# Performance work log

Measured on AMD Instinct MI355X. Metric: run time of the kernel, lower is better.

The kernel has to match this reference:

```python
import jax, jax.numpy as jnp
import numpy as np

N, E, F, H, L = 100000, 800000, 128, 128, 64


def _glorot(key, shape):
    lim = float(np.sqrt(6.0 / (shape[0] + shape[1])))
    return jax.random.uniform(key, shape, jnp.float32, -lim, lim)


def setup_inputs() -> dict:
    key = jax.random.key(0)
    ks = jax.random.split(key, 10)
    x = jax.random.normal(ks[0], (N, F), jnp.float32)
    noise = jax.random.normal(ks[1], (N, F), jnp.float32)
    edge_index = jax.random.randint(ks[2], (2, E), 0, N, jnp.int32)
    return {
        "x": x,
        "noise": noise,
        "edge_index": edge_index,
        "bn_gamma": jnp.ones((F,), jnp.float32),
        "bn_beta": jnp.zeros((F,), jnp.float32),
        "W1": _glorot(ks[3], (F, H)),
        "b1": jnp.zeros((H,), jnp.float32),
        "W2": _glorot(ks[4], (H + 2 * F, H)),
        "b2": jnp.zeros((H,), jnp.float32),
        "Wm": _glorot(ks[5], (H + F, L)),
        "bm": jnp.zeros((L,), jnp.float32),
        "Ws": _glorot(ks[6], (H + F, L)),
        "bs": jnp.zeros((L,), jnp.float32),
    }


def _gcn_conv(x, W, b, src, dst, norm, n):
    # GCNConv: transform, then sym-normalized sparse aggregation, then bias
    h = x @ W                                 # [n, out]
    msg = h[src] * norm[:, None]              # gather + scale  [E', out]
    return jax.ops.segment_sum(msg, dst, num_segments=n) + b


def reference(x, noise, edge_index, bn_gamma, bn_beta, W1, b1, W2, b2, Wm, bm, Ws, bs):
    n = x.shape[0]
    loops = jnp.arange(n, dtype=edge_index.dtype)
    src = jnp.concatenate([edge_index[0], loops])  # add self-loops
    dst = jnp.concatenate([edge_index[1], loops])
    deg = jax.ops.segment_sum(jnp.ones_like(src, dtype=x.dtype), dst, num_segments=n)
    dinv = jnp.where(deg > 0, jax.lax.rsqrt(jnp.maximum(deg, 1e-12)), 0.0)
    norm = dinv[src] * dinv[dst]                   # D^-1/2 A D^-1/2 edge weights

    # bn1 (training-mode batch norm over nodes)
    mu = x.mean(axis=0)
    var = x.var(axis=0)
    xb = (x - mu) * jax.lax.rsqrt(var + 1e-5) * bn_gamma + bn_beta

    h1 = jax.nn.relu(_gcn_conv(xb, W1, b1, src, dst, norm, n))
    h1 = jnp.concatenate([xb, noise, h1], axis=1)  # [n, H + 2F]
    h2 = jax.nn.relu(_gcn_conv(h1, W2, b2, src, dst, norm, n))
    # dropout(p=0.4) in eval mode -> identity
    last = jnp.concatenate([xb, h2], axis=1)       # [n, F + H]
    z_mean = _gcn_conv(last, Wm, bm, src, dst, norm, n)
    z_logstd = _gcn_conv(last, Ws, bs, src, dst, norm, n)
    return (z_mean, z_logstd)
```

## Files before the change

kernel.cpp:

```cpp
#include <hip/hip_runtime.h>
#include <math.h>


typedef short bf16x8 __attribute__((ext_vector_type(8)));
typedef float f32x4 __attribute__((ext_vector_type(4)));
typedef float f32x2 __attribute__((ext_vector_type(2)));

#define BN_G 1024
#define SCAN_BLK 256
#define SCAN_ELEMS 1024

__device__ inline unsigned short f2bf(float f) {
    unsigned int u = __builtin_bit_cast(unsigned int, f);
    u += 0x7fff + ((u >> 16) & 1);
    return (unsigned short)(u >> 16);
}
__device__ inline unsigned int pack2(float lo, float hi) {
    return ((unsigned int)f2bf(hi) << 16) | f2bf(lo);
}
__device__ inline f32x2 unp(unsigned int u) {
    return (f32x2){__builtin_bit_cast(float, u << 16),
                   __builtin_bit_cast(float, u & 0xffff0000u)};
}
__device__ inline void acc8v(f32x2* a, uint4 v) {
    a[0] += unp(v.x); a[1] += unp(v.y); a[2] += unp(v.z); a[3] += unp(v.w);
}

__device__ __forceinline__ void gload_lds16(const void* g, void* l) {
    __builtin_amdgcn_global_load_lds(
        (const __attribute__((address_space(1))) unsigned int*)g,
        (__attribute__((address_space(3))) unsigned int*)l, 16, 0, 0);
}

__global__ __launch_bounds__(256) void fused1(const float4* __restrict__ x4,
                                              float* __restrict__ partials, int n,
                                              const int* __restrict__ ei,
                                              int* __restrict__ cnt,
                                              int* __restrict__ slot, int E) {
    __shared__ float4 lds[2][8][32];
    int bid = blockIdx.x, t = threadIdx.x;
    if (bid < BN_G) {
        int cg = t & 31;
        int rs = t >> 5;
        float4 s = make_float4(0.f, 0.f, 0.f, 0.f);
        float4 q = make_float4(0.f, 0.f, 0.f, 0.f);
        const float4 z4 = make_float4(0.f, 0.f, 0.f, 0.f);
        const int stride = BN_G * 32;
        for (int r0 = bid * 32 + rs * 4; r0 < n; r0 += stride) {
            float4 v0 = x4[(size_t)r0 * 32 + cg];
            float4 v1 = (r0 + 1 < n) ? x4[(size_t)(r0 + 1) * 32 + cg] : z4;
            float4 v2 = (r0 + 2 < n) ? x4[(size_t)(r0 + 2) * 32 + cg] : z4;
            float4 v3 = (r0 + 3 < n) ? x4[(size_t)(r0 + 3) * 32 + cg] : z4;
            s.x += v0.x + v1.x + v2.x + v3.x;
            s.y += v0.y + v1.y + v2.y + v3.y;
            s.z += v0.z + v1.z + v2.z + v3.z;
            s.w += v0.w + v1.w + v2.w + v3.w;
            q.x = fmaf(v0.x, v0.x, fmaf(v1.x, v1.x, fmaf(v2.x, v2.x, fmaf(v3.x, v3.x, q.x))));
            q.y = fmaf(v0.y, v0.y, fmaf(v1.y, v1.y, fmaf(v2.y, v2.y, fmaf(v3.y, v3.y, q.y))));
            q.z = fmaf(v0.z, v0.z, fmaf(v1.z, v1.z, fmaf(v2.z, v2.z, fmaf(v3.z, v3.z, q.z))));
            q.w = fmaf(v0.w, v0.w, fmaf(v1.w, v1.w, fmaf(v2.w, v2.w, fmaf(v3.w, v3.w, q.w))));
        }
        lds[0][rs][cg] = s;
        lds[1][rs][cg] = q;
        __syncthreads();
        if (t < 64) {
            int which = t >> 5;
            int c = t & 31;
            float4 a = lds[which][0][c];
#pragma unroll
            for (int i = 1; i < 8; i++) {
                float4 b = lds[which][i][c];
                a.x += b.x; a.y += b.y; a.z += b.z; a.w += b.w;
            }
            int base = which * 128 + c * 4;
            partials[(size_t)(base + 0) * BN_G + bid] = a.x;
            partials[(size_t)(base + 1) * BN_G + bid] = a.y;
            partials[(size_t)(base + 2) * BN_G + bid] = a.z;
            partials[(size_t)(base + 3) * BN_G + bid] = a.w;
        }
        return;
    }
    int e = (bid - BN_G) * 256 + t;
    if (e < E) slot[e] = atomicAdd(&cnt[ei[E + e]], 1);
}

__global__ __launch_bounds__(256) void fused2(const float4* __restrict__ partials4,
                                              float* __restrict__ stats,
                                              const int* __restrict__ cnt,
                                              int* __restrict__ row_ptr,
                                              int* __restrict__ bsums, int n) {
    __shared__ float red[256];
    __shared__ int lds[SCAN_BLK];
    int t = threadIdx.x;
    if (blockIdx.x < 256) {
        int c = blockIdx.x;
        float4 v = partials4[(size_t)c * (BN_G / 4) + t];
        red[t] = v.x + v.y + v.z + v.w;
        __syncthreads();
        for (int off = 128; off > 0; off >>= 1) {
            if (t < off) red[t] += red[t + off];
            __syncthreads();
        }
        if (t == 0) stats[c] = red[0];
    } else {
        int blk = blockIdx.x - 256;
        int base = blk * SCAN_ELEMS;
        int v[4];
        int s = 0;
#pragma unroll
        for (int j = 0; j < 4; j++) {
            int i = base + t * 4 + j;
            v[j] = s;
            s += (i < n) ? cnt[i] : 0;
        }
        lds[t] = s;
        __syncthreads();
        for (int off = 1; off < SCAN_BLK; off <<= 1) {
            int val = (t >= off) ? lds[t - off] : 0;
            __syncthreads();
            lds[t] += val;
            __syncthreads();
        }
        int excl = (t == 0) ? 0 : lds[t - 1];
#pragma unroll
        for (int j = 0; j < 4; j++) {
            int i = base + t * 4 + j;
            if (i < n) row_ptr[i] = excl + v[j];
        }
        if (t == SCAN_BLK - 1) bsums[blk] = lds[t];
    }
}

__global__ void fused3(int* __restrict__ bsums, int nb,
                       const float* __restrict__ stats,
                       const float* __restrict__ gamma, const float* __restrict__ beta,
                       float* __restrict__ scale, float* __restrict__ shift, float invN) {
    int t = threadIdx.x;
    if (t == 0) {
        int acc = 0;
        for (int i = 0; i < nb; i++) { int c = bsums[i]; bsums[i] = acc; acc += c; }
    } else if (t >= 128 && t < 256) {
        int c = t - 128;
        float mu = stats[c] * invN;
        float var = stats[128 + c] * invN - mu * mu;
        float sc = gamma[c] / sqrtf(var + 1e-5f);
        scale[c] = sc;
        shift[c] = beta[c] - mu * sc;
    }
}

__global__ void fused4(int* __restrict__ row_ptr, const int* __restrict__ bsums,
                       const int* __restrict__ cnt, float* __restrict__ dinv,
                       int n, int E) {
    int i = blockIdx.x * blockDim.x + threadIdx.x;
    if (i < n) {
        row_ptr[i] += bsums[i / SCAN_ELEMS];
        dinv[i] = rsqrtf((float)cnt[i] + 1.0f);
    }
    if (i == 0) row_ptr[n] = E;
}

__device__ inline void pack_body(int i, const float* __restrict__ W,
                                 unsigned short* __restrict__ Wp,
                                 int K, int C, int colOff) {
    if (i >= K * C) return;
    int k = i / C, c = i % C;
    int gc = c + colOff;
    int s = k >> 7, kc = (k >> 5) & 3, lhi = (k >> 3) & 3, j = k & 7;
    int wc = gc >> 6, n = (gc >> 4) & 3, l15 = gc & 15;
    int lane = lhi * 16 + l15;
    size_t dst = ((size_t)((s * 2 + wc) * 4 + kc) * 4 + n) * 512 + lane * 8 + j;
    Wp[dst] = f2bf(W[i]);
}

__global__ __launch_bounds__(256) void fused5(
    const int* __restrict__ ei, const int* __restrict__ row_ptr,
    const int* __restrict__ slot, int* __restrict__ edge_src, int E, int EB,
    const float4* __restrict__ x4, const float4* __restrict__ n4,
    const float* __restrict__ scale, const float* __restrict__ shift,
    ushort4* __restrict__ xb, ushort4* __restrict__ nb4, int total4, int CB,
    const float* __restrict__ W1, unsigned short* __restrict__ Wp1,
    const float* __restrict__ W2, unsigned short* __restrict__ Wp2,
    const float* __restrict__ Wm, const float* __restrict__ Ws,
    unsigned short* __restrict__ Wpc)
{
    int bid = blockIdx.x, t = threadIdx.x;
    if (bid < EB) {
        int e = bid * 256 + t;
        if (e < E) {
            int s = ei[e], d = ei[E + e];
            edge_src[row_ptr[d] + slot[e]] = s;
        }
        return;
    }
    bid -= EB;
    if (bid < CB) {
        int i = bid * 256 + t;
        if (i < total4) {
            int c4 = (i & 31) << 2;
            float4 sc = *reinterpret_cast<const float4*>(scale + c4);
            float4 sh = *reinterpret_cast<const float4*>(shift + c4);
            float4 v = x4[i];
            ushort4 o;
            o.x = f2bf(fmaf(v.x, sc.x, sh.x));
            o.y = f2bf(fmaf(v.y, sc.y, sh.y));
            o.z = f2bf(fmaf(v.z, sc.z, sh.z));
            o.w = f2bf(fmaf(v.w, sc.w, sh.w));
            xb[i] = o;
            float4 w = n4[i];
            ushort4 p;
            p.x = f2bf(w.x); p.y = f2bf(w.y); p.z = f2bf(w.z); p.w = f2bf(w.w);
            nb4[i] = p;
        }
        return;
    }
    bid -= CB;
    if (bid < 64)  { pack_body(bid * 256 + t, W1, Wp1, 128, 128, 0); return; }
    bid -= 64;
    if (bid < 192) { pack_body(bid * 256 + t, W2, Wp2, 384, 128, 0); return; }
    bid -= 192;
    if (bid < 64)  { pack_body(bid * 256 + t, Wm, Wpc, 256, 64, 0); return; }
    bid -= 64;
    pack_body(bid * 256 + t, Ws, Wpc, 256, 64, 64);
}

template <int NSRC>
__global__ __launch_bounds__(256, 4) void gemm_mfma(
    const unsigned short* __restrict__ A0, const unsigned short* __restrict__ A1,
    const unsigned short* __restrict__ A2,
    const unsigned short* __restrict__ Wpk,
    const float* __restrict__ dinv, unsigned short* __restrict__ out)
{
    constexpr int NBUF = (NSRC > 1) ? 2 : 1;
    __shared__ unsigned char ldsA[NBUF][64 * 256];

    const int lane = threadIdx.x & 63;
    const int wid  = threadIdx.x >> 6;
    const int wr   = wid >> 1, wc = wid & 1;
    const int l15  = lane & 15, lhi = lane >> 4;
    const int c0   = wc * 64;
    const long rowblk = (long)blockIdx.x * 64;
    const int rl0 = wr * 32 + l15;
    const int rl1 = rl0 + 16;
    const int rsw = rl0 & 7;

    const unsigned short* __restrict__ srcs[3] = {A0, A1, A2};
    auto stage = [&](int s, int b) {
#pragma unroll
        for (int i = 0; i < 4; i++) {
            int G = (wid * 4 + i) * 64 + lane;
            int r = G >> 4, g = G & 15;
            const unsigned short* src = srcs[s] + (rowblk + r) * 128 + (g ^ (r & 7)) * 8;
            gload_lds16(src, &ldsA[b][G * 16]);
        }
    };

    f32x4 acc[2][4];
#pragma unroll
    for (int g = 0; g < 2; g++)
#pragma unroll
        for (int n = 0; n < 4; n++)
            acc[g][n] = (f32x4){0.f, 0.f, 0.f, 0.f};

    stage(0, 0);

#pragma unroll
    for (int s = 0; s < NSRC; s++) {
        const unsigned short* wbase = Wpk + ((size_t)(s * 2 + wc) * 16) * 512 + lane * 8;
        bf16x8 w[4][4];
#pragma unroll
        for (int kc = 0; kc < 4; kc++)
#pragma unroll
            for (int n = 0; n < 4; n++)
                w[kc][n] = *reinterpret_cast<const bf16x8*>(wbase + (kc * 4 + n) * 512);

        __syncthreads();
        if (s + 1 < NSRC) stage(s + 1, (s + 1) % NBUF);
        const unsigned char* bufp = ldsA[s % NBUF];

#pragma unroll
        for (int kc = 0; kc < 4; kc++) {
            int g0 = kc * 4 + lhi;
            bf16x8 a0 = *reinterpret_cast<const bf16x8*>(bufp + rl0 * 256 + (g0 ^ rsw) * 16);
            bf16x8 a1 = *reinterpret_cast<const bf16x8*>(bufp + rl1 * 256 + (g0 ^ rsw) * 16);
#pragma unroll
            for (int n = 0; n < 4; n++) {
                acc[0][n] = __builtin_amdgcn_mfma_f32_16x16x32_bf16(w[kc][n], a0, acc[0][n], 0, 0, 0);
                acc[1][n] = __builtin_amdgcn_mfma_f32_16x16x32_bf16(w[kc][n], a1, acc[1][n], 0, 0, 0);
            }
        }
    }

#pragma unroll
    for (int g = 0; g < 2; g++) {
        long row = rowblk + (g ? rl1 : rl0);
        float dv = dinv[row];
        unsigned short* op = out + row * 128 + c0 + lhi * 4;
#pragma unroll
        for (int n = 0; n < 4; n++) {
            f32x4 v = acc[g][n];
            ushort4 pk;
            pk.x = f2bf(v[0] * dv);
            pk.y = f2bf(v[1] * dv);
            pk.z = f2bf(v[2] * dv);
            pk.w = f2bf(v[3] * dv);
            *reinterpret_cast<ushort4*>(op + n * 16) = pk;
        }
    }
}

template <bool RELU>
__global__ void gather16(const uint4* __restrict__ hs4, const float* __restrict__ dinv,
                         const int* __restrict__ row_ptr, const int* __restrict__ edge_src,
                         const float* __restrict__ bias, uint4* __restrict__ out4, int n) {
    int node = blockIdx.x * 16 + (threadIdx.x >> 4);
    if (node >= n) return;
    int cl = threadIdx.x & 15;
    int beg = row_ptr[node], end = row_ptr[node + 1];
    f32x2 a[4] = {(f32x2){0.f,0.f}, (f32x2){0.f,0.f}, (f32x2){0.f,0.f}, (f32x2){0.f,0.f}};
    f32x2 b[4] = {(f32x2){0.f,0.f}, (f32x2){0.f,0.f}, (f32x2){0.f,0.f}, (f32x2){0.f,0.f}};
    acc8v(a, hs4[(size_t)node * 16 + cl]);
    int e = beg;
    for (; e + 4 <= end; e += 4) {
        uint4 v0 = hs4[(size_t)edge_src[e] * 16 + cl];
        uint4 v1 = hs4[(size_t)edge_src[e + 1] * 16 + cl];
        uint4 v2 = hs4[(size_t)edge_src[e + 2] * 16 + cl];
        uint4 v3 = hs4[(size_t)edge_src[e + 3] * 16 + cl];
        acc8v(a, v0);
        acc8v(b, v1);
        acc8v(a, v2);
        acc8v(b, v3);
    }
    if (e + 2 <= end) {
        uint4 v0 = hs4[(size_t)edge_src[e] * 16 + cl];
        uint4 v1 = hs4[(size_t)edge_src[e + 1] * 16 + cl];
        acc8v(a, v0);
        acc8v(b, v1);
        e += 2;
    }
    if (e < end) acc8v(a, hs4[(size_t)edge_src[e] * 16 + cl]);
#pragma unroll
    for (int i = 0; i < 4; i++) a[i] += b[i];
    float dv = dinv[node];
    float4 b0 = *reinterpret_cast<const float4*>(bias + cl * 8);
    float4 b1 = *reinterpret_cast<const float4*>(bias + cl * 8 + 4);
    float r0 = fmaf(a[0].x, dv, b0.x), r1 = fmaf(a[0].y, dv, b0.y);
    float r2 = fmaf(a[1].x, dv, b0.z), r3 = fmaf(a[1].y, dv, b0.w);
    float r4 = fmaf(a[2].x, dv, b1.x), r5 = fmaf(a[2].y, dv, b1.y);
    float r6 = fmaf(a[3].x, dv, b1.z), r7 = fmaf(a[3].y, dv, b1.w);
    if (RELU) {
        r0 = fmaxf(r0, 0.f); r1 = fmaxf(r1, 0.f); r2 = fmaxf(r2, 0.f); r3 = fmaxf(r3, 0.f);
        r4 = fmaxf(r4, 0.f); r5 = fmaxf(r5, 0.f); r6 = fmaxf(r6, 0.f); r7 = fmaxf(r7, 0.f);
    }
    uint4 o;
    o.x = pack2(r0, r1); o.y = pack2(r2, r3);
    o.z = pack2(r4, r5); o.w = pack2(r6, r7);
    out4[(size_t)node * 16 + cl] = o;
}

__global__ void gather_dual(const uint4* __restrict__ hs4, const float* __restrict__ dinv,
                            const int* __restrict__ row_ptr, const int* __restrict__ edge_src,
                            const float* __restrict__ bm, const float* __restrict__ bs,
                            float* __restrict__ zm, float* __restrict__ zs, int n) {
    int node = blockIdx.x * 16 + (threadIdx.x >> 4);
    if (node >= n) return;
    int cl = threadIdx.x & 15;
    int beg = row_ptr[node], end = row_ptr[node + 1];
    f32x2 a[4] = {(f32x2){0.f,0.f}, (f32x2){0.f,0.f}, (f32x2){0.f,0.f}, (f32x2){0.f,0.f}};
    f32x2 b[4] = {(f32x2){0.f,0.f}, (f32x2){0.f,0.f}, (f32x2){0.f,0.f}, (f32x2){0.f,0.f}};
    acc8v(a, hs4[(size_t)node * 16 + cl]);
    int e = beg;
    for (; e + 4 <= end; e += 4) {
        uint4 v0 = hs4[(size_t)edge_src[e] * 16 + cl];
        uint4 v1 = hs4[(size_t)edge_src[e + 1] * 16 + cl];
        uint4 v2 = hs4[(size_t)edge_src[e + 2] * 16 + cl];
        uint4 v3 = hs4[(size_t)edge_src[e + 3] * 16 + cl];
        acc8v(a, v0);
        acc8v(b, v1);
        acc8v(a, v2);
        acc8v(b, v3);
    }
    if (e + 2 <= end) {
        uint4 v0 = hs4[(size_t)edge_src[e] * 16 + cl];
        uint4 v1 = hs4[(size_t)edge_src[e + 1] * 16 + cl];
        acc8v(a, v0);
        acc8v(b, v1);
        e += 2;
    }
    if (e < end) acc8v(a, hs4[(size_t)edge_src[e] * 16 + cl]);
#pragma unroll
    for (int i = 0; i < 4; i++) a[i] += b[i];
    float dv = dinv[node];
    const float* bp = (cl < 8) ? (bm + cl * 8) : (bs + (cl - 8) * 8);
    float* zp = (cl < 8) ? (zm + (size_t)node * 64 + cl * 8)
                         : (zs + (size_t)node * 64 + (cl - 8) * 8);
    float4 b0 = *reinterpret_cast<const float4*>(bp);
    float4 b1 = *reinterpret_cast<const float4*>(bp + 4);
    float4 o0 = make_float4(fmaf(a[0].x, dv, b0.x), fmaf(a[0].y, dv, b0.y),
                            fmaf(a[1].x, dv, b0.z), fmaf(a[1].y, dv, b0.w));
    float4 o1 = make_float4(fmaf(a[2].x, dv, b1.x), fmaf(a[2].y, dv, b1.y),
                            fmaf(a[3].x, dv, b1.z), fmaf(a[3].y, dv, b1.w));
    *reinterpret_cast<float4*>(zp) = o0;
    *reinterpret_cast<float4*>(zp + 4) = o1;
}


extern "C" void kernel_launch(void* const* d_in, const int* in_sizes, int n_in,
                              void* d_out, int out_size, void* d_ws, size_t ws_size,
                              hipStream_t stream) {
    const float* x     = (const float*)d_in[0];
    const float* noise = (const float*)d_in[1];
    const int*   ei    = (const int*)d_in[2];
    const float* gamma = (const float*)d_in[3];
    const float* beta  = (const float*)d_in[4];
    const float* W1    = (const float*)d_in[5];
    const float* b1    = (const float*)d_in[6];
    const float* W2    = (const float*)d_in[7];
    const float* b2    = (const float*)d_in[8];
    const float* Wm    = (const float*)d_in[9];
    const float* bm    = (const float*)d_in[10];
    const float* Ws    = (const float*)d_in[11];
    const float* bs    = (const float*)d_in[12];

    const int N  = in_sizes[0] / 128;
    const int E  = in_sizes[2] / 2;
    const int NPAD = (N + 127) & ~127;
    const int nb = (N + SCAN_ELEMS - 1) / SCAN_ELEMS;
    const int EB = (E + 255) / 256;
    const int CB = (N * 32 + 255) / 256;

    auto align256 = [](size_t b) { return (b + 255) & ~(size_t)255; };
    char* p = (char*)d_ws;
    int* cnt      = (int*)p;  p += align256((size_t)N * 4);
    int* row_ptr  = (int*)p;  p += align256((size_t)(N + 1) * 4);
    int* edge_src = (int*)p;  p += align256((size_t)E * 4);
    int* slot     = (int*)p;  p += align256((size_t)E * 4);
    int* bsums    = (int*)p;  p += align256((size_t)nb * 4);
    float* dinv   = (float*)p; p += align256((size_t)NPAD * 4);
    float* stats  = (float*)p; p += align256(512 * 4);
    float* bnpart = (float*)p; p += align256((size_t)256 * BN_G * 4);
    unsigned short* Wp1 = (unsigned short*)p; p += align256(128 * 128 * 2);
    unsigned short* Wp2 = (unsigned short*)p; p += align256(128 * 384 * 2);
    unsigned short* Wpc = (unsigned short*)p; p += align256(128 * 256 * 2);
    unsigned short* xb16 = (unsigned short*)p; p += align256((size_t)NPAD * 128 * 2);
    unsigned short* n16  = (unsigned short*)p; p += align256((size_t)NPAD * 128 * 2);
    unsigned short* h16  = (unsigned short*)p; p += align256((size_t)NPAD * 128 * 2);

    float* scale = stats + 256;
    float* shift = stats + 384;

    float* dout = (float*)d_out;
    unsigned short* hs12 = (unsigned short*)d_out;
    unsigned short* hs3  = n16;
    float* zm = dout;
    float* zs = dout + (size_t)N * 64;

    const int gblocks = NPAD / 64;
    const int nblocks16 = (N + 15) / 16;

    hipMemsetAsync(cnt, 0, (size_t)N * 4, stream);
    fused1<<<BN_G + EB, 256, 0, stream>>>((const float4*)x, bnpart, N, ei, cnt, slot, E);
    fused2<<<256 + nb, 256, 0, stream>>>((const float4*)bnpart, stats, cnt, row_ptr, bsums, N);
    fused3<<<1, 256, 0, stream>>>(bsums, nb, stats, gamma, beta, scale, shift, 1.0f / (float)N);
    fused4<<<(N + 255) / 256, 256, 0, stream>>>(row_ptr, bsums, cnt, dinv, N, E);
    fused5<<<EB + CB + 384, 256, 0, stream>>>(
        ei, row_ptr, slot, edge_src, E, EB,
        (const float4*)x, (const float4*)noise, scale, shift,
        (ushort4*)xb16, (ushort4*)n16, N * 32, CB,
        W1, Wp1, W2, Wp2, Wm, Ws, Wpc);

    gemm_mfma<1><<<gblocks, 256, 0, stream>>>(xb16, nullptr, nullptr, Wp1, dinv, hs12);
    gather16<true><<<nblocks16, 256, 0, stream>>>((const uint4*)hs12, dinv, row_ptr,
                                                  edge_src, b1, (uint4*)h16, N);
    gemm_mfma<3><<<gblocks, 256, 0, stream>>>(xb16, n16, h16, Wp2, dinv, hs12);
    gather16<true><<<nblocks16, 256, 0, stream>>>((const uint4*)hs12, dinv, row_ptr,
                                                  edge_src, b2, (uint4*)h16, N);
    gemm_mfma<2><<<gblocks, 256, 0, stream>>>(xb16, h16, nullptr, Wpc, dinv, hs3);
    gather_dual<<<nblocks16, 256, 0, stream>>>((const uint4*)hs3, dinv, row_ptr,
                                               edge_src, bm, bs, zm, zs, N);
}
```

Before: 272.6 us.

## Fuse sparse gather aggregation into following GEMM via LDS staging

Replaces the standalone gather16 kernels with a gather_gemm kernel. Each block first aggregates neighbor rows for its 64 nodes, applying bias and ReLU, and writes the result into swizzled LDS. It then feeds that tile directly into the MFMA GEMM with the other dense inputs. This removes a global-memory round trip of the intermediate h activations and two kernel launches. In exchange, the gather runs with only 64 rows per block, one thread group per four nodes serially, and higher LDS use, which may limit occupancy and latency hiding for the irregular gather.

```diff
diff --git a/kernel.cpp b/kernel.cpp
--- a/kernel.cpp
+++ b/kernel.cpp
@@ -309,53 +309,147 @@
     }
 }
 
-template <bool RELU>
-__global__ void gather16(const uint4* __restrict__ hs4, const float* __restrict__ dinv,
-                         const int* __restrict__ row_ptr, const int* __restrict__ edge_src,
-                         const float* __restrict__ bias, uint4* __restrict__ out4, int n) {
-    int node = blockIdx.x * 16 + (threadIdx.x >> 4);
-    if (node >= n) return;
-    int cl = threadIdx.x & 15;
-    int beg = row_ptr[node], end = row_ptr[node + 1];
-    f32x2 a[4] = {(f32x2){0.f,0.f}, (f32x2){0.f,0.f}, (f32x2){0.f,0.f}, (f32x2){0.f,0.f}};
-    f32x2 b[4] = {(f32x2){0.f,0.f}, (f32x2){0.f,0.f}, (f32x2){0.f,0.f}, (f32x2){0.f,0.f}};
-    acc8v(a, hs4[(size_t)node * 16 + cl]);
-    int e = beg;
-    for (; e + 4 <= end; e += 4) {
-        uint4 v0 = hs4[(size_t)edge_src[e] * 16 + cl];
-        uint4 v1 = hs4[(size_t)edge_src[e + 1] * 16 + cl];
-        uint4 v2 = hs4[(size_t)edge_src[e + 2] * 16 + cl];
-        uint4 v3 = hs4[(size_t)edge_src[e + 3] * 16 + cl];
-        acc8v(a, v0);
-        acc8v(b, v1);
-        acc8v(a, v2);
-        acc8v(b, v3);
-    }
-    if (e + 2 <= end) {
-        uint4 v0 = hs4[(size_t)edge_src[e] * 16 + cl];
-        uint4 v1 = hs4[(size_t)edge_src[e + 1] * 16 + cl];
-        acc8v(a, v0);
-        acc8v(b, v1);
-        e += 2;
-    }
-    if (e < end) acc8v(a, hs4[(size_t)edge_src[e] * 16 + cl]);
-#pragma unroll
-    for (int i = 0; i < 4; i++) a[i] += b[i];
-    float dv = dinv[node];
-    float4 b0 = *reinterpret_cast<const float4*>(bias + cl * 8);
-    float4 b1 = *reinterpret_cast<const float4*>(bias + cl * 8 + 4);
-    float r0 = fmaf(a[0].x, dv, b0.x), r1 = fmaf(a[0].y, dv, b0.y);
-    float r2 = fmaf(a[1].x, dv, b0.z), r3 = fmaf(a[1].y, dv, b0.w);
-    float r4 = fmaf(a[2].x, dv, b1.x), r5 = fmaf(a[2].y, dv, b1.y);
-    float r6 = fmaf(a[3].x, dv, b1.z), r7 = fmaf(a[3].y, dv, b1.w);
-    if (RELU) {
-        r0 = fmaxf(r0, 0.f); r1 = fmaxf(r1, 0.f); r2 = fmaxf(r2, 0.f); r3 = fmaxf(r3, 0.f);
-        r4 = fmaxf(r4, 0.f); r5 = fmaxf(r5, 0.f); r6 = fmaxf(r6, 0.f); r7 = fmaxf(r7, 0.f);
-    }
-    uint4 o;
-    o.x = pack2(r0, r1); o.y = pack2(r2, r3);
-    o.z = pack2(r4, r5); o.w = pack2(r6, r7);
-    out4[(size_t)node * 16 + cl] = o;
+template <int NG>
+__global__ __launch_bounds__(256, 3) void gather_gemm(
+    const unsigned short* __restrict__ A0, const unsigned short* __restrict__ A1,
+    const uint4* __restrict__ hsrc,
+    const float* __restrict__ dinv, const int* __restrict__ row_ptr,
+    const int* __restrict__ edge_src, const float* __restrict__ gbias,
+    const unsigned short* __restrict__ Wpk,
+    unsigned short* __restrict__ out, int n)
+{
+    constexpr int NSRC = NG + 1;
+    __shared__ unsigned char ldsA[NG][64 * 256];
+    __shared__ uint4 hlds[64 * 16];
+
+    const int t = threadIdx.x;
+    const int lane = t & 63;
+    const int wid  = t >> 6;
+    const int wr   = wid >> 1, wc = wid & 1;
+    const int l15  = lane & 15, lhi = lane >> 4;
+    const int c0   = wc * 64;
+    const long rowblk = (long)blockIdx.x * 64;
+    const int rl0 = wr * 32 + l15;
+    const int rl1 = rl0 + 16;
+    const int rsw = rl0 & 7;
+
+    const unsigned short* __restrict__ srcs[2] = {A0, A1};
+    auto stage = [&](int s, int b) {
+#pragma unroll
+        for (int i = 0; i < 4; i++) {
+            int G = (wid * 4 + i) * 64 + lane;
+            int r = G >> 4, g = G & 15;
+            const unsigned short* src = srcs[s] + (rowblk + r) * 128 + (g ^ (r & 7)) * 8;
+            gload_lds16(src, &ldsA[b][G * 16]);
+        }
+    };
+
+    stage(0, 0);
+
+    {
+        int grp = t >> 4, cl = t & 15;
+#pragma unroll
+        for (int i = 0; i < 4; i++) {
+            int r = grp * 4 + i;
+            long node = rowblk + r;
+            uint4 o = make_uint4(0u, 0u, 0u, 0u);
+            if (node < n) {
+                int beg = row_ptr[node], end = row_ptr[node + 1];
+                f32x2 a[4] = {(f32x2){0.f,0.f}, (f32x2){0.f,0.f},
+                              (f32x2){0.f,0.f}, (f32x2){0.f,0.f}};
+                f32x2 ab[4] = {(f32x2){0.f,0.f}, (f32x2){0.f,0.f},
+                               (f32x2){0.f,0.f}, (f32x2){0.f,0.f}};
+                acc8v(a, hsrc[(size_t)node * 16 + cl]);
+                int e = beg;
+                for (; e + 4 <= end; e += 4) {
+                    uint4 v0 = hsrc[(size_t)edge_src[e] * 16 + cl];
+                    uint4 v1 = hsrc[(size_t)edge_src[e + 1] * 16 + cl];
+                    uint4 v2 = hsrc[(size_t)edge_src[e + 2] * 16 + cl];
+                    uint4 v3 = hsrc[(size_t)edge_src[e + 3] * 16 + cl];
+                    acc8v(a, v0);
+                    acc8v(ab, v1);
+                    acc8v(a, v2);
+                    acc8v(ab, v3);
+                }
+                if (e + 2 <= end) {
+                    uint4 v0 = hsrc[(size_t)edge_src[e] * 16 + cl];
+                    uint4 v1 = hsrc[(size_t)edge_src[e + 1] * 16 + cl];
+                    acc8v(a, v0);
+                    acc8v(ab, v1);
+                    e += 2;
+                }
+                if (e < end) acc8v(a, hsrc[(size_t)edge_src[e] * 16 + cl]);
+#pragma unroll
+                for (int j = 0; j < 4; j++) a[j] += ab[j];
+                float dv = dinv[node];
+                float4 b0 = *reinterpret_cast<const float4*>(gbias + cl * 8);
+                float4 b1 = *reinterpret_cast<const float4*>(gbias + cl * 8 + 4);
+                float r0 = fmaxf(fmaf(a[0].x, dv, b0.x), 0.f);
+                float r1 = fmaxf(fmaf(a[0].y, dv, b0.y), 0.f);
+                float r2 = fmaxf(fmaf(a[1].x, dv, b0.z), 0.f);
+                float r3 = fmaxf(fmaf(a[1].y, dv, b0.w), 0.f);
+                float r4 = fmaxf(fmaf(a[2].x, dv, b1.x), 0.f);
+                float r5 = fmaxf(fmaf(a[2].y, dv, b1.y), 0.f);
+                float r6 = fmaxf(fmaf(a[3].x, dv, b1.z), 0.f);
+                float r7 = fmaxf(fmaf(a[3].y, dv, b1.w), 0.f);
+                o.x = pack2(r0, r1); o.y = pack2(r2, r3);
+                o.z = pack2(r4, r5); o.w = pack2(r6, r7);
+            }
+            hlds[r * 16 + (cl ^ (r & 7))] = o;
+        }
+    }
+
+    f32x4 acc[2][4];
+#pragma unroll
+    for (int g = 0; g < 2; g++)
+#pragma unroll
+        for (int n = 0; n < 4; n++)
+            acc[g][n] = (f32x4){0.f, 0.f, 0.f, 0.f};
+
+#pragma unroll
+    for (int s = 0; s < NSRC; s++) {
+        const unsigned short* wbase = Wpk + ((size_t)(s * 2 + wc) * 16) * 512 + lane * 8;
+        bf16x8 w[4][4];
+#pragma unroll
+        for (int kc = 0; kc < 4; kc++)
+#pragma unroll
+            for (int n = 0; n < 4; n++)
+                w[kc][n] = *reinterpret_cast<const bf16x8*>(wbase + (kc * 4 + n) * 512);
+
+        __syncthreads();
+        if (s + 1 < NG) stage(s + 1, s + 1);
+        const unsigned char* bufp = (s < NG) ? ldsA[s]
+                                             : reinterpret_cast<const unsigned char*>(hlds);
+
+#pragma unroll
+        for (int kc = 0; kc < 4; kc++) {
+            int g0 = kc * 4 + lhi;
+            bf16x8 a0 = *reinterpret_cast<const bf16x8*>(bufp + rl0 * 256 + (g0 ^ rsw) * 16);
+            bf16x8 a1 = *reinterpret_cast<const bf16x8*>(bufp + rl1 * 256 + (g0 ^ rsw) * 16);
+#pragma unroll
+            for (int n = 0; n < 4; n++) {
+                acc[0][n] = __builtin_amdgcn_mfma_f32_16x16x32_bf16(w[kc][n], a0, acc[0][n], 0, 0, 0);
+                acc[1][n] = __builtin_amdgcn_mfma_f32_16x16x32_bf16(w[kc][n], a1, acc[1][n], 0, 0, 0);
+            }
+        }
+    }
+
+#pragma unroll
+    for (int g = 0; g < 2; g++) {
+        long row = rowblk + (g ? rl1 : rl0);
+        float dv = dinv[row];
+        unsigned short* op = out + row * 128 + c0 + lhi * 4;
+#pragma unroll
+        for (int n = 0; n < 4; n++) {
+            f32x4 v = acc[g][n];
+            ushort4 pk;
+            pk.x = f2bf(v[0] * dv);
+            pk.y = f2bf(v[1] * dv);
+            pk.z = f2bf(v[2] * dv);
+            pk.w = f2bf(v[3] * dv);
+            *reinterpret_cast<ushort4*>(op + n * 16) = pk;
+        }
+    }
 }
 
 __global__ void gather_dual(const uint4* __restrict__ hs4, const float* __restrict__ dinv,
@@ -451,7 +545,6 @@
 
     float* dout = (float*)d_out;
     unsigned short* hs12 = (unsigned short*)d_out;
-    unsigned short* hs3  = n16;
     float* zm = dout;
     float* zs = dout + (size_t)N * 64;
 
@@ -469,13 +562,11 @@
         (ushort4*)xb16, (ushort4*)n16, N * 32, CB,
         W1, Wp1, W2, Wp2, Wm, Ws, Wpc);
 
-    gemm_mfma<1><<<gblocks, 256, 0, stream>>>(xb16, nullptr, nullptr, Wp1, dinv, hs12);
-    gather16<true><<<nblocks16, 256, 0, stream>>>((const uint4*)hs12, dinv, row_ptr,
-                                                  edge_src, b1, (uint4*)h16, N);
-    gemm_mfma<3><<<gblocks, 256, 0, stream>>>(xb16, n16, h16, Wp2, dinv, hs12);
-    gather16<true><<<nblocks16, 256, 0, stream>>>((const uint4*)hs12, dinv, row_ptr,
-                                                  edge_src, b2, (uint4*)h16, N);
-    gemm_mfma<2><<<gblocks, 256, 0, stream>>>(xb16, h16, nullptr, Wpc, dinv, hs3);
-    gather_dual<<<nblocks16, 256, 0, stream>>>((const uint4*)hs3, dinv, row_ptr,
+    gemm_mfma<1><<<gblocks, 256, 0, stream>>>(xb16, nullptr, nullptr, Wp1, dinv, h16);
+    gather_gemm<2><<<gblocks, 256, 0, stream>>>(
+        xb16, n16, (const uint4*)h16, dinv, row_ptr, edge_src, b1, Wp2, hs12, N);
+    gather_gemm<1><<<gblocks, 256, 0, stream>>>(
+        xb16, nullptr, (const uint4*)hs12, dinv, row_ptr, edge_src, b2, Wpc, h16, N);
+    gather_dual<<<nblocks16, 256, 0, stream>>>((const uint4*)h16, dinv, row_ptr,
                                                edge_src, bm, bs, zm, zs, N);
 }
```

Measured after the change: 293.5 us. +7.7%, slower.

## Fold batch-norm affine into weights and GEMM epilogue; convert raw x early

Applied to the files above, without the earlier changes.

Batch-norm scale is folded into the rows of each packed weight matrix that multiply the xb block. The shift term becomes a per-column bias vector (shift·W), computed by three extra blocks and added in the GEMM epilogue. Raw x is converted to bf16 inside the stats pass while it is already loaded, so the later pass that re-read x in fp32 to normalize it is removed. The cost is rounding the unnormalized x to bf16 instead of the normalized values, which may shift precision, plus extra stores in the stats kernel.

```diff
diff --git a/kernel.cpp b/kernel.cpp
--- a/kernel.cpp
+++ b/kernel.cpp
@@ -25,6 +25,11 @@
 __device__ inline void acc8v(f32x2* a, uint4 v) {
     a[0] += unp(v.x); a[1] += unp(v.y); a[2] += unp(v.z); a[3] += unp(v.w);
 }
+__device__ inline ushort4 cvt4(float4 v) {
+    ushort4 o;
+    o.x = f2bf(v.x); o.y = f2bf(v.y); o.z = f2bf(v.z); o.w = f2bf(v.w);
+    return o;
+}
 
 __device__ __forceinline__ void gload_lds16(const void* g, void* l) {
     __builtin_amdgcn_global_load_lds(
@@ -34,6 +39,7 @@
 
 __global__ __launch_bounds__(256) void fused1(const float4* __restrict__ x4,
                                               float* __restrict__ partials, int n,
+                                              ushort4* __restrict__ x16,
                                               const int* __restrict__ ei,
                                               int* __restrict__ cnt,
                                               int* __restrict__ slot, int E) {
@@ -51,6 +57,10 @@
             float4 v1 = (r0 + 1 < n) ? x4[(size_t)(r0 + 1) * 32 + cg] : z4;
             float4 v2 = (r0 + 2 < n) ? x4[(size_t)(r0 + 2) * 32 + cg] : z4;
             float4 v3 = (r0 + 3 < n) ? x4[(size_t)(r0 + 3) * 32 + cg] : z4;
+            x16[(size_t)r0 * 32 + cg] = cvt4(v0);
+            if (r0 + 1 < n) x16[(size_t)(r0 + 1) * 32 + cg] = cvt4(v1);
+            if (r0 + 2 < n) x16[(size_t)(r0 + 2) * 32 + cg] = cvt4(v2);
+            if (r0 + 3 < n) x16[(size_t)(r0 + 3) * 32 + cg] = cvt4(v3);
             s.x += v0.x + v1.x + v2.x + v3.x;
             s.y += v0.y + v1.y + v2.y + v3.y;
             s.z += v0.z + v1.z + v2.z + v3.z;
@@ -162,28 +172,32 @@
 
 __device__ inline void pack_body(int i, const float* __restrict__ W,
                                  unsigned short* __restrict__ Wp,
-                                 int K, int C, int colOff) {
+                                 int K, int C, int colOff,
+                                 const float* __restrict__ scale) {
     if (i >= K * C) return;
     int k = i / C, c = i % C;
+    float v = W[i];
+    if (k < 128) v *= scale[k];
     int gc = c + colOff;
     int s = k >> 7, kc = (k >> 5) & 3, lhi = (k >> 3) & 3, j = k & 7;
     int wc = gc >> 6, n = (gc >> 4) & 3, l15 = gc & 15;
     int lane = lhi * 16 + l15;
     size_t dst = ((size_t)((s * 2 + wc) * 4 + kc) * 4 + n) * 512 + lane * 8 + j;
-    Wp[dst] = f2bf(W[i]);
+    Wp[dst] = f2bf(v);
 }
 
 __global__ __launch_bounds__(256) void fused5(
     const int* __restrict__ ei, const int* __restrict__ row_ptr,
     const int* __restrict__ slot, int* __restrict__ edge_src, int E, int EB,
-    const float4* __restrict__ x4, const float4* __restrict__ n4,
+    const float4* __restrict__ n4, ushort4* __restrict__ nb4, int total4, int CB,
     const float* __restrict__ scale, const float* __restrict__ shift,
-    ushort4* __restrict__ xb, ushort4* __restrict__ nb4, int total4, int CB,
     const float* __restrict__ W1, unsigned short* __restrict__ Wp1,
     const float* __restrict__ W2, unsigned short* __restrict__ Wp2,
     const float* __restrict__ Wm, const float* __restrict__ Ws,
-    unsigned short* __restrict__ Wpc)
+    unsigned short* __restrict__ Wpc,
+    float* __restrict__ cv1, float* __restrict__ cv2, float* __restrict__ cvc)
 {
+    __shared__ float cred[256];
     int bid = blockIdx.x, t = threadIdx.x;
     if (bid < EB) {
         int e = bid * 256 + t;
@@ -196,32 +210,41 @@
     bid -= EB;
     if (bid < CB) {
         int i = bid * 256 + t;
-        if (i < total4) {
-            int c4 = (i & 31) << 2;
-            float4 sc = *reinterpret_cast<const float4*>(scale + c4);
-            float4 sh = *reinterpret_cast<const float4*>(shift + c4);
-            float4 v = x4[i];
-            ushort4 o;
-            o.x = f2bf(fmaf(v.x, sc.x, sh.x));
-            o.y = f2bf(fmaf(v.y, sc.y, sh.y));
-            o.z = f2bf(fmaf(v.z, sc.z, sh.z));
-            o.w = f2bf(fmaf(v.w, sc.w, sh.w));
-            xb[i] = o;
-            float4 w = n4[i];
-            ushort4 p;
-            p.x = f2bf(w.x); p.y = f2bf(w.y); p.z = f2bf(w.z); p.w = f2bf(w.w);
-            nb4[i] = p;
-        }
+        if (i < total4) nb4[i] = cvt4(n4[i]);
         return;
     }
     bid -= CB;
-    if (bid < 64)  { pack_body(bid * 256 + t, W1, Wp1, 128, 128, 0); return; }
+    if (bid < 64)  { pack_body(bid * 256 + t, W1, Wp1, 128, 128, 0, scale); return; }
     bid -= 64;
-    if (bid < 192) { pack_body(bid * 256 + t, W2, Wp2, 384, 128, 0); return; }
+    if (bid < 192) { pack_body(bid * 256 + t, W2, Wp2, 384, 128, 0, scale); return; }
     bid -= 192;
-    if (bid < 64)  { pack_body(bid * 256 + t, Wm, Wpc, 256, 64, 0); return; }
+    if (bid < 64)  { pack_body(bid * 256 + t, Wm, Wpc, 256, 64, 0, scale); return; }
     bid -= 64;
-    pack_body(bid * 256 + t, Ws, Wpc, 256, 64, 64);
+    if (bid < 64)  { pack_body(bid * 256 + t, Ws, Wpc, 256, 64, 64, scale); return; }
+    bid -= 64;
+    {
+        int c = t & 127, kh = t >> 7;
+        float s = 0.f;
+        if (bid == 0) {
+            for (int k = kh * 64; k < kh * 64 + 64; k++)
+                s = fmaf(shift[k], W1[k * 128 + c], s);
+        } else if (bid == 1) {
+            for (int k = kh * 64; k < kh * 64 + 64; k++)
+                s = fmaf(shift[k], W2[k * 128 + c], s);
+        } else {
+            const float* Wsrc = (c < 64) ? Wm : Ws;
+            int cc = (c < 64) ? c : c - 64;
+            for (int k = kh * 64; k < kh * 64 + 64; k++)
+                s = fmaf(shift[k], Wsrc[k * 64 + cc], s);
+        }
+        cred[t] = s;
+        __syncthreads();
+        if (t < 128) {
+            float v = cred[t] + cred[t + 128];
+            float* dst = (bid == 0) ? cv1 : (bid == 1) ? cv2 : cvc;
+            dst[c] = v;
+        }
+    }
 }
 
 template <int NSRC>
@@ -229,7 +252,8 @@
     const unsigned short* __restrict__ A0, const unsigned short* __restrict__ A1,
     const unsigned short* __restrict__ A2,
     const unsigned short* __restrict__ Wpk,
-    const float* __restrict__ dinv, unsigned short* __restrict__ out)
+    const float* __restrict__ dinv, const float* __restrict__ cvec,
+    unsigned short* __restrict__ out)
 {
     constexpr int NBUF = (NSRC > 1) ? 2 : 1;
     __shared__ unsigned char ldsA[NBUF][64 * 256];
@@ -291,6 +315,11 @@
         }
     }
 
+    float4 cv[4];
+#pragma unroll
+    for (int n = 0; n < 4; n++)
+        cv[n] = *reinterpret_cast<const float4*>(cvec + c0 + n * 16 + lhi * 4);
+
 #pragma unroll
     for (int g = 0; g < 2; g++) {
         long row = rowblk + (g ? rl1 : rl0);
@@ -300,10 +329,10 @@
         for (int n = 0; n < 4; n++) {
             f32x4 v = acc[g][n];
             ushort4 pk;
-            pk.x = f2bf(v[0] * dv);
-            pk.y = f2bf(v[1] * dv);
-            pk.z = f2bf(v[2] * dv);
-            pk.w = f2bf(v[3] * dv);
+            pk.x = f2bf((v[0] + cv[n].x) * dv);
+            pk.y = f2bf((v[1] + cv[n].y) * dv);
+            pk.z = f2bf((v[2] + cv[n].z) * dv);
+            pk.w = f2bf((v[3] + cv[n].w) * dv);
             *reinterpret_cast<ushort4*>(op + n * 16) = pk;
         }
     }
@@ -438,13 +467,16 @@
     int* bsums    = (int*)p;  p += align256((size_t)nb * 4);
     float* dinv   = (float*)p; p += align256((size_t)NPAD * 4);
     float* stats  = (float*)p; p += align256(512 * 4);
+    float* cv1    = (float*)p; p += align256(128 * 4);
+    float* cv2    = (float*)p; p += align256(128 * 4);
+    float* cvc    = (float*)p; p += align256(128 * 4);
     float* bnpart = (float*)p; p += align256((size_t)256 * BN_G * 4);
     unsigned short* Wp1 = (unsigned short*)p; p += align256(128 * 128 * 2);
     unsigned short* Wp2 = (unsigned short*)p; p += align256(128 * 384 * 2);
     unsigned short* Wpc = (unsigned short*)p; p += align256(128 * 256 * 2);
-    unsigned short* xb16 = (unsigned short*)p; p += align256((size_t)NPAD * 128 * 2);
-    unsigned short* n16  = (unsigned short*)p; p += align256((size_t)NPAD * 128 * 2);
-    unsigned short* h16  = (unsigned short*)p; p += align256((size_t)NPAD * 128 * 2);
+    unsigned short* x16 = (unsigned short*)p; p += align256((size_t)NPAD * 128 * 2);
+    unsigned short* n16 = (unsigned short*)p; p += align256((size_t)NPAD * 128 * 2);
+    unsigned short* h16 = (unsigned short*)p; p += align256((size_t)NPAD * 128 * 2);
 
     float* scale = stats + 256;
     float* shift = stats + 384;
@@ -459,23 +491,23 @@
     const int nblocks16 = (N + 15) / 16;
 
     hipMemsetAsync(cnt, 0, (size_t)N * 4, stream);
-    fused1<<<BN_G + EB, 256, 0, stream>>>((const float4*)x, bnpart, N, ei, cnt, slot, E);
+    fused1<<<BN_G + EB, 256, 0, stream>>>((const float4*)x, bnpart, N,
+                                          (ushort4*)x16, ei, cnt, slot, E);
     fused2<<<256 + nb, 256, 0, stream>>>((const float4*)bnpart, stats, cnt, row_ptr, bsums, N);
     fused3<<<1, 256, 0, stream>>>(bsums, nb, stats, gamma, beta, scale, shift, 1.0f / (float)N);
     fused4<<<(N + 255) / 256, 256, 0, stream>>>(row_ptr, bsums, cnt, dinv, N, E);
-    fused5<<<EB + CB + 384, 256, 0, stream>>>(
+    fused5<<<EB + CB + 384 + 3, 256, 0, stream>>>(
         ei, row_ptr, slot, edge_src, E, EB,
-        (const float4*)x, (const float4*)noise, scale, shift,
-        (ushort4*)xb16, (ushort4*)n16, N * 32, CB,
-        W1, Wp1, W2, Wp2, Wm, Ws, Wpc);
-
-    gemm_mfma<1><<<gblocks, 256, 0, stream>>>(xb16, nullptr, nullptr, Wp1, dinv, hs12);
+        (const float4*)noise, (ushort4*)n16, N * 32, CB,
+        scale, shift, W1, Wp1, W2, Wp2, Wm, Ws, Wpc, cv1, cv2, cvc);
+
+    gemm_mfma<1><<<gblocks, 256, 0, stream>>>(x16, nullptr, nullptr, Wp1, dinv, cv1, hs12);
     gather16<true><<<nblocks16, 256, 0, stream>>>((const uint4*)hs12, dinv, row_ptr,
                                                   edge_src, b1, (uint4*)h16, N);
-    gemm_mfma<3><<<gblocks, 256, 0, stream>>>(xb16, n16, h16, Wp2, dinv, hs12);
+    gemm_mfma<3><<<gblocks, 256, 0, stream>>>(x16, n16, h16, Wp2, dinv, cv2, hs12);
     gather16<true><<<nblocks16, 256, 0, stream>>>((const uint4*)hs12, dinv, row_ptr,
                                                   edge_src, b2, (uint4*)h16, N);
-    gemm_mfma<2><<<gblocks, 256, 0, stream>>>(xb16, h16, nullptr, Wpc, dinv, hs3);
+    gemm_mfma<2><<<gblocks, 256, 0, stream>>>(x16, h16, nullptr, Wpc, dinv, cvc, hs3);
     gather_dual<<<nblocks16, 256, 0, stream>>>((const uint4*)hs3, dinv, row_ptr,
                                                edge_src, bm, bs, zm, zs, N);
 }
```

Result: no change. 272.6 us, median of 2 (+0.0%).
